# Kernel tuning notes

Hardware: AMD Instinct MI355X
Metric: run time of the kernel (lower is better)

The kernel has to match this reference:

```python
import jax, jax.numpy as jnp
import numpy as np

P = 8.0  # Lp norm order for NormDist layers (finite-p distance conv)
CHUNK = 8  # output-channel chunk for memory-bounded distance computation
EPS = 8.0 / 255.0


def lp_norm(d, p=P):
    # stable Lp norm over last axis: m * (sum((d/m)^p))^(1/p)
    m = jnp.max(d, axis=-1)
    ms = jnp.where(m > 0, m, 1.0)
    s = jnp.sum((d / ms[..., None]) ** p, axis=-1)
    ss = jnp.where(m > 0, s, 1.0)
    return m * ss ** (1.0 / p)


def extract_patches(t, k, s, pad):
    # [B,C,H,W] -> [B, L, C*k*k] (torch-unfold channel-major ordering), L=Ho*Wo
    pt = jax.lax.conv_general_dilated_patches(t, (k, k), (s, s), [(pad, pad), (pad, pad)])
    B, F, Ho, Wo = pt.shape
    return pt.reshape(B, F, Ho * Wo).transpose(0, 2, 1), Ho, Wo


def normdist_conv(c, lo, hi, w, k, s, pad):
    # Lp-distance conv with interval bound propagation on (center, lower, upper)
    pc, Ho, Wo = extract_patches(c, k, s, pad)
    pl, _, _ = extract_patches(lo, k, s, pad)
    ph, _, _ = extract_patches(hi, k, s, pad)
    O = w.shape[0]
    wf = w.reshape(O, -1)  # [O, F]

    def per_chunk(wc):  # wc: [CHUNK, F]
        dc = jnp.abs(pc[:, :, None, :] - wc)                     # [B,L,CHUNK,F]
        oc = lp_norm(dc)
        # per-element distance bounds given lo <= x <= hi
        dl = jnp.maximum(jnp.maximum(pl[:, :, None, :] - wc, wc - ph[:, :, None, :]), 0.0)
        ol = lp_norm(dl)
        dh = jnp.maximum(jnp.abs(pl[:, :, None, :] - wc), jnp.abs(ph[:, :, None, :] - wc))
        oh = lp_norm(dh)
        return oc, ol, oh

    oc, ol, oh = jax.lax.map(per_chunk, wf.reshape(O // CHUNK, CHUNK, -1))

    def to_img(t):  # [nch, B, L, CHUNK] -> [B, O, Ho, Wo]
        nch, B, L, ch = t.shape
        return t.transpose(1, 0, 3, 2).reshape(B, nch * ch, Ho, Wo)

    return to_img(oc), to_img(ol), to_img(oh)


def bound_relu(c, lo, hi):
    return jax.nn.relu(c), jax.nn.relu(lo), jax.nn.relu(hi)


def _mp(t):
    return jax.lax.reduce_window(t, -jnp.inf, jax.lax.max, (1, 1, 3, 3), (1, 1, 2, 2), 'VALID')


def bound_maxpool(c, lo, hi):
    return _mp(c), _mp(lo), _mp(hi)


def bound_linear(c, lo, hi, W, b=None):
    oc = c @ W.T
    mid = ((lo + hi) * 0.5) @ W.T
    rad = ((hi - lo) * 0.5) @ jnp.abs(W).T
    if b is not None:
        oc = oc + b
        mid = mid + b
    return oc, mid - rad, mid + rad


def setup_inputs() -> dict:
    key = jax.random.key(0)
    ks = jax.random.split(key, 10)
    x = jax.random.normal(ks[0], (16, 3, 32, 32), jnp.float32)
    lower = x - EPS
    upper = x + EPS
    w1 = jax.random.normal(ks[1], (96, 3, 7, 7), jnp.float32)
    w2 = jax.random.normal(ks[2], (256, 96, 5, 5), jnp.float32)
    w3 = jax.random.normal(ks[3], (384, 256, 3, 3), jnp.float32)
    w4 = jax.random.normal(ks[4], (384, 384, 3, 3), jnp.float32)
    w5 = jax.random.normal(ks[5], (256, 384, 3, 3), jnp.float32)
    fw1 = jax.random.normal(ks[6], (1024, 2304), jnp.float32) * 0.02
    fw2 = jax.random.normal(ks[7], (512, 1024), jnp.float32) * 0.03
    fw3 = jax.random.normal(ks[8], (10, 512), jnp.float32) * 0.04
    fb3 = jax.random.normal(ks[9], (10,), jnp.float32)
    return {"x": x, "lower": lower, "upper": upper, "w1": w1, "w2": w2, "w3": w3,
            "w4": w4, "w5": w5, "fw1": fw1, "fw2": fw2, "fw3": fw3, "fb3": fb3}


def reference(x, lower, upper, w1, w2, w3, w4, w5, fw1, fw2, fw3, fb3):
    c, l, u = normdist_conv(x, lower, upper, w1, 7, 2, 2)   # 32 -> 15
    c, l, u = bound_relu(c, l, u)
    c, l, u = bound_maxpool(c, l, u)                        # 15 -> 7
    c, l, u = normdist_conv(c, l, u, w2, 5, 1, 2)           # 7 -> 7
    c, l, u = bound_relu(c, l, u)
    c, l, u = bound_maxpool(c, l, u)                        # 7 -> 3
    c, l, u = normdist_conv(c, l, u, w3, 3, 1, 1)
    c, l, u = bound_relu(c, l, u)
    c, l, u = normdist_conv(c, l, u, w4, 3, 1, 1)
    c, l, u = bound_relu(c, l, u)
    c, l, u = normdist_conv(c, l, u, w5, 3, 1, 1)
    c, l, u = bound_relu(c, l, u)
    B = c.shape[0]
    c, l, u = c.reshape(B, -1), l.reshape(B, -1), u.reshape(B, -1)
    c, l, u = bound_linear(c, l, u, fw1)
    c, l, u = bound_relu(c, l, u)
    c, l, u = bound_linear(c, l, u, fw2)
    c, l, u = bound_relu(c, l, u)
    c, l, u = bound_linear(c, l, u, fw3, fb3)
    # final negation swaps the roles of lower/upper
    return (-c, -u, -l)
```

## Files before the change

### kernel.cpp

```cpp
#include <hip/hip_runtime.h>
#include <math.h>


typedef float vf2 __attribute__((ext_vector_type(2)));

__device__ __forceinline__ float rt8(float s) { return sqrtf(sqrtf(sqrtf(s))); }

__device__ __forceinline__ void tap16(float w, float pc, float pl, float pu,
                                      float& aC, float& aL, float& aH)
{
    float a = pc - w; float a2 = a * a, a4 = a2 * a2; aC = fmaf(a4, a4, aC);
    float x = pl - w, y = pu - w;
    float dl = fmaxf(fmaxf(x, -y), 0.f);
    float e2 = dl * dl, e4 = e2 * e2; aL = fmaf(e4, e4, aL);
    float h2 = fmaxf(x * x, y * y);
    float h4 = h2 * h2; aH = fmaf(h4, h4, aH);
}

__device__ __forceinline__ void tap16v2(vf2 w, vf2 pc, vf2 pl, vf2 pu,
                                        vf2& aC, vf2& aL, vf2& aH)
{
    vf2 a = pc - w; vf2 a2 = a * a, a4 = a2 * a2;
    aC = __builtin_elementwise_fma(a4, a4, aC);
    vf2 x = pl - w, y = pu - w;
    vf2 zero = {0.f, 0.f};
    vf2 dl = __builtin_elementwise_max(__builtin_elementwise_max(x, -y), zero);
    vf2 e2 = dl * dl, e4 = e2 * e2;
    aL = __builtin_elementwise_fma(e4, e4, aL);
    vf2 h2 = __builtin_elementwise_max(x * x, y * y);
    vf2 h4 = h2 * h2;
    aH = __builtin_elementwise_fma(h4, h4, aH);
}

__launch_bounds__(256)
__global__ void prep_kernel(const float* __restrict__ W2, const float* __restrict__ W3,
                            const float* __restrict__ W4, const float* __restrict__ W5,
                            float* __restrict__ T2, float* __restrict__ T3,
                            float* __restrict__ T4, float* __restrict__ T5,
                            const float* __restrict__ IC, const float* __restrict__ IL,
                            const float* __restrict__ IU, const float* __restrict__ W1,
                            float* __restrict__ A)
{
    constexpr int nt2 = 152, nt3 = 216, nt4 = 324, nt5 = 216;
    constexpr int NTW = nt2 + nt3 + nt4 + nt5;
    __shared__ float u[3 * 3 * 1225];
    int bid = blockIdx.x;
    int tid = threadIdx.x;

    if (bid < NTW) {
        const float* W; float* T; int O, CK, KK, t;
        if (bid < nt2)                  { W = W2; T = T2; O = 256; CK = 2400; KK = 25; t = bid; }
        else if (bid < nt2 + nt3)       { W = W3; T = T3; O = 384; CK = 2304; KK = 9; t = bid - nt2; }
        else if (bid < nt2 + nt3 + nt4) { W = W4; T = T4; O = 384; CK = 3456; KK = 9; t = bid - nt2 - nt3; }
        else                            { W = W5; T = T5; O = 256; CK = 3456; KK = 9; t = bid - nt2 - nt3 - nt4; }
        int tilesC = (CK + 63) / 64;
        int to = t / tilesC, tc = t - to * tilesC;
        int o0 = to * 64, c0 = tc * 64;
        int lane = tid & 63, wv = tid >> 6;
        #pragma unroll
        for (int i = 0; i < 16; ++i) {
            int row = wv + i * 4;
            int c = c0 + lane;
            u[row * 65 + lane] = (c < CK) ? W[(size_t)(o0 + row) * CK + c] : 0.f;
        }
        __syncthreads();
        #pragma unroll
        for (int i = 0; i < 16; ++i) {
            int row = wv + i * 4;
            int ck = c0 + row;
            if (ck < CK) {
                int c = ck / KK, tt = ck - c * KK;
                T[(size_t)((c >> 1) * KK + tt) * (2 * O) + (size_t)(o0 + lane) * 2 + (c & 1)]
                    = u[lane * 65 + row];
            }
        }
        return;
    }

    constexpr int PP = 1225, PW = 35, HW = 1024;
    int t = bid - NTW;
    int og = t % 24; t /= 24;
    int b  = t % 16; int r = t / 16;

    for (int i = tid; i < 3 * 3 * PP; i += 256) u[i] = 0.f;
    __syncthreads();
    for (int tsel = 0; tsel < 3; ++tsel) {
        const float* src = (tsel == 0 ? IC : (tsel == 1 ? IL : IU)) + (size_t)b * 3 * HW;
        for (int e = tid; e < 3 * HW; e += 256) {
            int c = e / HW, p = e % HW;
            int pr = p / 32, pw_ = p % 32;
            u[c * 3 * PP + tsel * PP + (pr + 2) * PW + (pw_ + 2)] = src[e];
        }
    }
    __syncthreads();

    int wave = tid >> 6, lane = tid & 63;
    int o = og * 4 + wave;
    const float* wp = W1 + (size_t)o * 147;
    int pos = r * 64 + lane;
    if (pos < 225) {
        int oh = pos / 15, ow = pos % 15;
        const float* sl = u + (oh * 2) * PW + ow * 2;
        float aC = 0.f, aL = 0.f, aH = 0.f;
        #pragma unroll
        for (int c = 0; c < 3; ++c) {
            #pragma unroll
            for (int kh = 0; kh < 7; ++kh)
                #pragma unroll
                for (int kw = 0; kw < 7; ++kw) {
                    float w = wp[c * 49 + kh * 7 + kw];
                    tap16(w, sl[kh * PW + kw], sl[PP + kh * PW + kw],
                          sl[2 * PP + kh * PW + kw], aC, aL, aH);
                }
            sl += 3 * PP;
        }
        size_t N = (size_t)16 * 96 * 225;
        size_t oi = ((size_t)b * 96 + o) * 225 + pos;
        A[oi] = aC; A[N + oi] = aL; A[2 * N + oi] = aH;
    }
}

template<int CC>
__launch_bounds__(256)
__global__ void conv2_kernel(const float* __restrict__ A, const float* __restrict__ WT,
                             float* __restrict__ P)
{
    constexpr int B = 16, Cin = 96, O = 256;
    constexpr int CP = CC / 2;
    constexpr size_t N = (size_t)B * O * 49;
    constexpr size_t NA = (size_t)B * 96 * 225;
    __shared__ __align__(16) float slab[CP * 360];
    int x = blockIdx.x;
    int oh   = x % 7;
    int b    = (x / 7) % B;
    int chunk = x / (7 * B);
    int c0 = chunk * CC;
    int tid = threadIdx.x;

    for (int i = tid; i < CP * 360; i += 256) {
        int cp = i / 360; int rem = i - cp * 360;
        int tsel = rem / 120; int rr = rem - tsel * 120;
        int r = rr / 24; int cpar = rr - r * 24;
        int col = cpar >> 1, par = cpar & 1;
        int c = c0 + cp * 2 + par;
        int ih = oh + r - 2, iw = col - 2;
        float v = 0.f;
        if (col < 11 && (unsigned)ih < 7u && (unsigned)iw < 7u) {
            const float* ap = A + (size_t)tsel * NA + ((size_t)b * 96 + c) * 225
                            + (ih * 2) * 15 + iw * 2;
            float m = 0.f;
            #pragma unroll
            for (int pi = 0; pi < 3; ++pi)
                #pragma unroll
                for (int pj = 0; pj < 3; ++pj)
                    m = fmaxf(m, ap[pi * 15 + pj]);
            v = rt8(m);
        }
        slab[i] = v;
    }
    __syncthreads();

    int o = tid;
    vf2 aC2[7], aL2[7], aH2[7];
    vf2 zero = {0.f, 0.f};
    #pragma unroll
    for (int u = 0; u < 7; ++u) { aC2[u] = zero; aL2[u] = zero; aH2[u] = zero; }

    for (int cp = 0; cp < CP; ++cp) {
        const float* wp = WT + (size_t)((c0 / 2 + cp) * 25) * (2 * O) + 2 * o;
        const float* sb = slab + cp * 360;
        #pragma unroll
        for (int r = 0; r < 5; ++r) {
            vf2 wr[5];
            #pragma unroll
            for (int kw = 0; kw < 5; ++kw)
                wr[kw] = *(const vf2*)(wp + (size_t)(r * 5 + kw) * (2 * O));
            vf2 X[12], L[12], U[12];
            #pragma unroll
            for (int i2 = 0; i2 < 12; ++i2) {
                X[i2] = *(const vf2*)(sb + r * 24 + i2 * 2);
                L[i2] = *(const vf2*)(sb + 120 + r * 24 + i2 * 2);
                U[i2] = *(const vf2*)(sb + 240 + r * 24 + i2 * 2);
            }
            #pragma unroll
            for (int ow = 0; ow < 7; ++ow)
                #pragma unroll
                for (int kw = 0; kw < 5; ++kw)
                    tap16v2(wr[kw], X[ow + kw], L[ow + kw], U[ow + kw],
                            aC2[ow], aL2[ow], aH2[ow]);
        }
    }

    float* Pc = P + (size_t)chunk * 3 * N;
    size_t rowbase = ((size_t)(b * 7 + oh) * 7) * O + o;
    #pragma unroll
    for (int u = 0; u < 7; ++u) {
        Pc[rowbase + (size_t)u * O]         = aC2[u].x + aC2[u].y;
        Pc[N + rowbase + (size_t)u * O]     = aL2[u].x + aL2[u].y;
        Pc[2 * N + rowbase + (size_t)u * O] = aH2[u].x + aH2[u].y;
    }
}

__global__ void comb2_pool2(const float* __restrict__ P, float* __restrict__ D)
{
    constexpr int B = 16, O = 256, NCH = 16;
    constexpr size_t N = (size_t)B * O * 49;
    int idx = blockIdx.x * blockDim.x + threadIdx.x;
    if (idx >= 3 * B * 9 * O) return;
    int o = idx & 255; int t = idx >> 8;
    int pos = t % 9; t /= 9;
    int b = t % B; int tsel = t / B;
    int ph = pos / 3, pw = pos % 3;
    float m = 0.f;
    #pragma unroll
    for (int i = 0; i < 3; ++i)
        #pragma unroll
        for (int j = 0; j < 3; ++j) {
            int sp = (ph * 2 + i) * 7 + (pw * 2 + j);
            size_t base = (size_t)tsel * N + ((size_t)b * 49 + sp) * O + o;
            float s = 0.f;
            #pragma unroll
            for (int ch = 0; ch < NCH; ++ch) s += P[(size_t)ch * 3 * N + base];
            m = fmaxf(m, s);
        }
    D[idx] = rt8(m);
}

template<int CC, int NCHIN>
__launch_bounds__(384)
__global__ void conv3x3_kernel(const float* __restrict__ IN, const float* __restrict__ WT,
                               float* __restrict__ P, int B, int Cin, int O)
{
    constexpr int CP = CC / 2;
    __shared__ __align__(8) float slab[CP * 150];
    int x = blockIdx.x;
    int b = x % B;
    int chunk = x / B;
    int c0 = chunk * CC;
    int tid = threadIdx.x;

    size_t NN = (size_t)B * Cin * 9;
    for (int i = tid; i < CP * 150; i += blockDim.x) {
        int cp = i / 150; int rem = i - cp * 150;
        int tsel = rem / 50; int rr = rem - tsel * 50;
        int p = rr >> 1, par = rr & 1;
        int iy = p / 5, ix = p - iy * 5;
        int ih = iy - 1, iw = ix - 1;
        int c = c0 + cp * 2 + par;
        float v = 0.f;
        if ((unsigned)ih < 3u && (unsigned)iw < 3u) {
            size_t base = (size_t)tsel * NN + ((size_t)b * 9 + (ih * 3 + iw)) * Cin + c;
            if (NCHIN == 0) {
                v = IN[base];
            } else {
                float s = 0.f;
                #pragma unroll 8
                for (int ch = 0; ch < NCHIN; ++ch) s += IN[(size_t)ch * 3 * NN + base];
                v = rt8(s);
            }
        }
        slab[i] = v;
    }
    __syncthreads();

    int o = tid;
    vf2 aC2[9], aL2[9], aH2[9];
    vf2 zero = {0.f, 0.f};
    #pragma unroll
    for (int u = 0; u < 9; ++u) { aC2[u] = zero; aL2[u] = zero; aH2[u] = zero; }

    for (int cp = 0; cp < CP; ++cp) {
        const float* wp = WT + (size_t)((c0 / 2 + cp) * 9) * (2 * O) + 2 * o;
        vf2 w2[9];
        #pragma unroll
        for (int t = 0; t < 9; ++t) w2[t] = *(const vf2*)(wp + (size_t)t * (2 * O));
        const float* sb = slab + cp * 150;
        #pragma unroll
        for (int py = 0; py < 3; ++py)
            #pragma unroll
            for (int px = 0; px < 3; ++px)
                #pragma unroll
                for (int ky = 0; ky < 3; ++ky)
                    #pragma unroll
                    for (int kx = 0; kx < 3; ++kx) {
                        int p = (py + ky) * 5 + (px + kx);
                        tap16v2(w2[ky * 3 + kx],
                                *(const vf2*)(sb + p * 2),
                                *(const vf2*)(sb + 50 + p * 2),
                                *(const vf2*)(sb + 100 + p * 2),
                                aC2[py * 3 + px], aL2[py * 3 + px], aH2[py * 3 + px]);
                    }
    }

    size_t N = (size_t)B * O * 9;
    float* Pc = P + (size_t)chunk * 3 * N;
    size_t base = ((size_t)b * 9) * O + o;
    #pragma unroll
    for (int u = 0; u < 9; ++u) {
        Pc[base + (size_t)u * O]         = aC2[u].x + aC2[u].y;
        Pc[N + base + (size_t)u * O]     = aL2[u].x + aL2[u].y;
        Pc[2 * N + base + (size_t)u * O] = aH2[u].x + aH2[u].y;
    }
}

__global__ void comb5_std(const float* __restrict__ P, float* __restrict__ G, int NCH)
{
    constexpr int B = 16, O = 256;
    constexpr size_t N = (size_t)B * O * 9;
    size_t idx = (size_t)blockIdx.x * blockDim.x + threadIdx.x;
    if (idx >= 3 * N) return;
    float s = 0.f;
    for (int ch = 0; ch < NCH; ++ch) s += P[(size_t)ch * 3 * N + idx];
    int o = (int)(idx % O); size_t t = idx / O;
    int pos = (int)(t % 9); t /= 9;
    int b = (int)(t % B); int tsel = (int)(t / B);
    G[(size_t)tsel * N + ((size_t)b * O + o) * 9 + pos] = rt8(s);
}

__launch_bounds__(256)
__global__ void fc_gemv(const float* __restrict__ IC, const float* __restrict__ IL,
                        const float* __restrict__ IU, const float* __restrict__ W,
                        float* __restrict__ OUT, int B, int In, int Out)
{
    int gw = (int)((blockIdx.x * blockDim.x + threadIdx.x) >> 6);
    int lane = threadIdx.x & 63;
    if (gw >= B * Out) return;
    int o = gw % Out, b = gw / Out;
    const float4* wr = (const float4*)(W  + (size_t)o * In);
    const float4* cr = (const float4*)(IC + (size_t)b * In);
    const float4* lr = (const float4*)(IL + (size_t)b * In);
    const float4* ur = (const float4*)(IU + (size_t)b * In);
    int In4 = In >> 2;
    float sc = 0.f, sm = 0.f, sr = 0.f;
    for (int i = lane; i < In4; i += 64) {
        float4 w4 = wr[i], c4 = cr[i], l4 = lr[i], u4 = ur[i];
        sc = fmaf(c4.x, w4.x, sc); sc = fmaf(c4.y, w4.y, sc);
        sc = fmaf(c4.z, w4.z, sc); sc = fmaf(c4.w, w4.w, sc);
        sm = fmaf((l4.x + u4.x) * 0.5f, w4.x, sm);
        sm = fmaf((l4.y + u4.y) * 0.5f, w4.y, sm);
        sm = fmaf((l4.z + u4.z) * 0.5f, w4.z, sm);
        sm = fmaf((l4.w + u4.w) * 0.5f, w4.w, sm);
        sr = fmaf((u4.x - l4.x) * 0.5f, fabsf(w4.x), sr);
        sr = fmaf((u4.y - l4.y) * 0.5f, fabsf(w4.y), sr);
        sr = fmaf((u4.z - l4.z) * 0.5f, fabsf(w4.z), sr);
        sr = fmaf((u4.w - l4.w) * 0.5f, fabsf(w4.w), sr);
    }
    #pragma unroll
    for (int off = 32; off; off >>= 1) {
        sc += __shfl_xor(sc, off);
        sm += __shfl_xor(sm, off);
        sr += __shfl_xor(sr, off);
    }
    if (lane == 0) {
        size_t N = (size_t)B * Out;
        size_t idx = (size_t)b * Out + o;
        OUT[idx]         = fmaxf(sc, 0.f);
        OUT[N + idx]     = fmaxf(sm - sr, 0.f);
        OUT[2 * N + idx] = fmaxf(sm + sr, 0.f);
    }
}

__global__ void bound_linear_kernel(
    const float* __restrict__ IC, const float* __restrict__ IL, const float* __restrict__ IU,
    const float* __restrict__ W, const float* __restrict__ bias,
    float* __restrict__ OC, float* __restrict__ OL, float* __restrict__ OU,
    int B, int In, int Out)
{
    int idx = blockIdx.x * blockDim.x + threadIdx.x;
    if (idx >= B * Out) return;
    int o = idx % Out, b = idx / Out;
    const float* wr = W  + (size_t)o * In;
    const float* cr = IC + (size_t)b * In;
    const float* lr = IL + (size_t)b * In;
    const float* ur = IU + (size_t)b * In;
    float sc = 0.f, sm = 0.f, sr = 0.f;
    for (int i = 0; i < In; ++i) {
        float w = wr[i];
        sc = fmaf(cr[i], w, sc);
        sm = fmaf((lr[i] + ur[i]) * 0.5f, w, sm);
        sr = fmaf((ur[i] - lr[i]) * 0.5f, fabsf(w), sr);
    }
    float bb = bias[o]; sc += bb; sm += bb;
    OC[idx] = -sc; OL[idx] = -(sm - sr); OU[idx] = -(sm + sr);
}

extern "C" void kernel_launch(void* const* d_in, const int* in_sizes, int n_in,
                              void* d_out, int out_size, void* d_ws, size_t ws_size,
                              hipStream_t stream)
{
    const float* x   = (const float*)d_in[0];
    const float* lo  = (const float*)d_in[1];
    const float* hi  = (const float*)d_in[2];
    const float* w1  = (const float*)d_in[3];
    const float* w2  = (const float*)d_in[4];
    const float* w3  = (const float*)d_in[5];
    const float* w4  = (const float*)d_in[6];
    const float* w5  = (const float*)d_in[7];
    const float* fw1 = (const float*)d_in[8];
    const float* fw2 = (const float*)d_in[9];
    const float* fw3 = (const float*)d_in[10];
    const float* fb3 = (const float*)d_in[11];
    float* out = (float*)d_out;
    float* ws  = (float*)d_ws;

    const size_t n_c1 = 16u * 96 * 225;
    const size_t n_d  = 16u * 256 * 9;
    const size_t n_c5 = 16u * 256 * 9;
    const size_t n_f1 = 16u * 1024;
    const size_t n_f2 = 16u * 512;
    const size_t N3   = 16u * 384 * 9;

    float* A   = ws;
    float* D   = A  + 3 * n_c1;
    float* G   = D  + 3 * n_d;
    float* H   = G  + 3 * n_c5;
    float* I   = H  + 3 * n_f1;
    float* WT2 = I  + 3 * n_f2;
    float* WT3 = WT2 + 614400;
    float* WT4 = WT3 + 884736;
    float* WT5 = WT4 + 1327104;
    float* SP2 = WT5 + 884736;
    float* SPa = SP2;
    float* SPc = SP2;
    float* SPb = SP2 + 32u * 3 * N3;

    const int BS = 256;
    auto grid = [](size_t tot) { return dim3((unsigned)((tot + 255) / 256)); };

    prep_kernel<<<908 + 1536, BS, 0, stream>>>(
        w2, w3, w4, w5, WT2, WT3, WT4, WT5, x, lo, hi, w1, A);
    conv2_kernel<6><<<16 * 16 * 7, 256, 0, stream>>>(A, WT2, SP2);
    comb2_pool2<<<grid(3 * n_d), BS, 0, stream>>>(SP2, D);
    conv3x3_kernel<8, 0><<<32 * 16, 384, 0, stream>>>(D, WT3, SPa, 16, 256, 384);
    conv3x3_kernel<8, 32><<<48 * 16, 384, 0, stream>>>(SPa, WT4, SPb, 16, 384, 384);
    conv3x3_kernel<8, 48><<<48 * 16, 256, 0, stream>>>(SPb, WT5, SPc, 16, 384, 256);
    comb5_std<<<grid(3 * n_c5), BS, 0, stream>>>(SPc, G, 48);
    fc_gemv<<<grid(16384u * 64), BS, 0, stream>>>(
        G, G + n_c5, G + 2 * n_c5, fw1, H, 16, 2304, 1024);
    fc_gemv<<<grid(8192u * 64), BS, 0, stream>>>(
        H, H + n_f1, H + 2 * n_f1, fw2, I, 16, 1024, 512);
    bound_linear_kernel<<<grid(160), BS, 0, stream>>>(
        I, I + n_f2, I + 2 * n_f2, fw3, fb3,
        out, out + 320, out + 160, 16, 512, 10);
}
```

Before: 582.5 us.

## Fuse pool into conv3, register-tile 3x3 slab, batch FC gemv, retune conv2 chunks

```diff
diff --git a/kernel.cpp b/kernel.cpp
--- a/kernel.cpp
+++ b/kernel.cpp
@@ -201,38 +201,29 @@
     }
 }
 
-__global__ void comb2_pool2(const float* __restrict__ P, float* __restrict__ D)
-{
-    constexpr int B = 16, O = 256, NCH = 16;
-    constexpr size_t N = (size_t)B * O * 49;
-    int idx = blockIdx.x * blockDim.x + threadIdx.x;
-    if (idx >= 3 * B * 9 * O) return;
-    int o = idx & 255; int t = idx >> 8;
-    int pos = t % 9; t /= 9;
-    int b = t % B; int tsel = t / B;
-    int ph = pos / 3, pw = pos % 3;
-    float m = 0.f;
-    #pragma unroll
-    for (int i = 0; i < 3; ++i)
-        #pragma unroll
-        for (int j = 0; j < 3; ++j) {
-            int sp = (ph * 2 + i) * 7 + (pw * 2 + j);
-            size_t base = (size_t)tsel * N + ((size_t)b * 49 + sp) * O + o;
-            float s = 0.f;
-            #pragma unroll
-            for (int ch = 0; ch < NCH; ++ch) s += P[(size_t)ch * 3 * N + base];
-            m = fmaxf(m, s);
-        }
-    D[idx] = rt8(m);
-}
-
-template<int CC, int NCHIN>
+#define LDROW(R, off, iy) { \
+    float4 q0 = *(const float4*)(sb + (off) + (iy) * 12); \
+    float4 q1 = *(const float4*)(sb + (off) + (iy) * 12 + 4); \
+    vf2   q2 = *(const vf2*)(sb + (off) + (iy) * 12 + 8); \
+    R[iy][0] = vf2{q0.x, q0.y}; R[iy][1] = vf2{q0.z, q0.w}; \
+    R[iy][2] = vf2{q1.x, q1.y}; R[iy][3] = vf2{q1.z, q1.w}; \
+    R[iy][4] = q2; }
+
+#define TAPS(py) \
+    _Pragma("unroll") for (int px = 0; px < 3; ++px) \
+    _Pragma("unroll") for (int ky = 0; ky < 3; ++ky) \
+    _Pragma("unroll") for (int kx = 0; kx < 3; ++kx) \
+        tap16v2(w2[ky * 3 + kx], X[(py) + ky][px + kx], L[(py) + ky][px + kx], \
+                U[(py) + ky][px + kx], aC2[(py) * 3 + px], aL2[(py) * 3 + px], \
+                aH2[(py) * 3 + px]);
+
+template<int CC, int NCHIN, bool POOL>
 __launch_bounds__(384)
 __global__ void conv3x3_kernel(const float* __restrict__ IN, const float* __restrict__ WT,
                                float* __restrict__ P, int B, int Cin, int O)
 {
     constexpr int CP = CC / 2;
-    __shared__ __align__(8) float slab[CP * 150];
+    __shared__ __align__(16) float slab[CP * 180];
     int x = blockIdx.x;
     int b = x % B;
     int chunk = x / B;
@@ -240,19 +231,34 @@
     int tid = threadIdx.x;
 
     size_t NN = (size_t)B * Cin * 9;
-    for (int i = tid; i < CP * 150; i += blockDim.x) {
-        int cp = i / 150; int rem = i - cp * 150;
-        int tsel = rem / 50; int rr = rem - tsel * 50;
-        int p = rr >> 1, par = rr & 1;
-        int iy = p / 5, ix = p - iy * 5;
-        int ih = iy - 1, iw = ix - 1;
+    constexpr size_t N2 = (size_t)16 * 256 * 49;
+    for (int i = tid; i < CP * 180; i += blockDim.x) {
+        int cp = i / 180; int rem = i - cp * 180;
+        int tsel = rem / 60; int rr = rem - tsel * 60;
+        int iy = rr / 12; int cc2 = rr - iy * 12;
+        int col = cc2 >> 1, par = cc2 & 1;
+        int ih = iy - 1, iw = col - 1;
         int c = c0 + cp * 2 + par;
         float v = 0.f;
         if ((unsigned)ih < 3u && (unsigned)iw < 3u) {
-            size_t base = (size_t)tsel * NN + ((size_t)b * 9 + (ih * 3 + iw)) * Cin + c;
-            if (NCHIN == 0) {
-                v = IN[base];
+            if (POOL) {
+                float m = 0.f;
+                #pragma unroll
+                for (int pi = 0; pi < 3; ++pi)
+                    #pragma unroll
+                    for (int pj = 0; pj < 3; ++pj) {
+                        int sp = (ih * 2 + pi) * 7 + (iw * 2 + pj);
+                        size_t base = (size_t)tsel * N2 + ((size_t)b * 49 + sp) * 256 + c;
+                        float s = 0.f;
+                        #pragma unroll
+                        for (int ch = 0; ch < 12; ++ch) s += IN[(size_t)ch * 3 * N2 + base];
+                        m = fmaxf(m, s);
+                    }
+                v = rt8(m);
+            } else if (NCHIN == 0) {
+                v = IN[(size_t)tsel * NN + ((size_t)b * 9 + (ih * 3 + iw)) * Cin + c];
             } else {
+                size_t base = (size_t)tsel * NN + ((size_t)b * 9 + (ih * 3 + iw)) * Cin + c;
                 float s = 0.f;
                 #pragma unroll 8
                 for (int ch = 0; ch < NCHIN; ++ch) s += IN[(size_t)ch * 3 * NN + base];
@@ -274,22 +280,16 @@
         vf2 w2[9];
         #pragma unroll
         for (int t = 0; t < 9; ++t) w2[t] = *(const vf2*)(wp + (size_t)t * (2 * O));
-        const float* sb = slab + cp * 150;
-        #pragma unroll
-        for (int py = 0; py < 3; ++py)
-            #pragma unroll
-            for (int px = 0; px < 3; ++px)
-                #pragma unroll
-                for (int ky = 0; ky < 3; ++ky)
-                    #pragma unroll
-                    for (int kx = 0; kx < 3; ++kx) {
-                        int p = (py + ky) * 5 + (px + kx);
-                        tap16v2(w2[ky * 3 + kx],
-                                *(const vf2*)(sb + p * 2),
-                                *(const vf2*)(sb + 50 + p * 2),
-                                *(const vf2*)(sb + 100 + p * 2),
-                                aC2[py * 3 + px], aL2[py * 3 + px], aH2[py * 3 + px]);
-                    }
+        const float* sb = slab + cp * 180;
+        vf2 X[5][5], L[5][5], U[5][5];
+        LDROW(X, 0, 0) LDROW(L, 60, 0) LDROW(U, 120, 0)
+        LDROW(X, 0, 1) LDROW(L, 60, 1) LDROW(U, 120, 1)
+        LDROW(X, 0, 2) LDROW(L, 60, 2) LDROW(U, 120, 2)
+        TAPS(0)
+        LDROW(X, 0, 3) LDROW(L, 60, 3) LDROW(U, 120, 3)
+        TAPS(1)
+        LDROW(X, 0, 4) LDROW(L, 60, 4) LDROW(U, 120, 4)
+        TAPS(2)
     }
 
     size_t N = (size_t)B * O * 9;
@@ -318,45 +318,64 @@
 }
 
 __launch_bounds__(256)
-__global__ void fc_gemv(const float* __restrict__ IC, const float* __restrict__ IL,
-                        const float* __restrict__ IU, const float* __restrict__ W,
-                        float* __restrict__ OUT, int B, int In, int Out)
-{
+__global__ void fc_gemv4(const float* __restrict__ IC, const float* __restrict__ IL,
+                         const float* __restrict__ IU, const float* __restrict__ W,
+                         float* __restrict__ OUT, int In, int Out)
+{
+    constexpr int B = 16;
     int gw = (int)((blockIdx.x * blockDim.x + threadIdx.x) >> 6);
     int lane = threadIdx.x & 63;
-    if (gw >= B * Out) return;
-    int o = gw % Out, b = gw / Out;
-    const float4* wr = (const float4*)(W  + (size_t)o * In);
-    const float4* cr = (const float4*)(IC + (size_t)b * In);
-    const float4* lr = (const float4*)(IL + (size_t)b * In);
-    const float4* ur = (const float4*)(IU + (size_t)b * In);
+    if (gw >= Out * 4) return;
+    int o = gw % Out, bg = gw / Out;
+    int b0 = bg * 4;
+    const float4* wr = (const float4*)(W + (size_t)o * In);
+    const float4* cr[4]; const float4* lr[4]; const float4* ur[4];
+    #pragma unroll
+    for (int q = 0; q < 4; ++q) {
+        cr[q] = (const float4*)(IC + (size_t)(b0 + q) * In);
+        lr[q] = (const float4*)(IL + (size_t)(b0 + q) * In);
+        ur[q] = (const float4*)(IU + (size_t)(b0 + q) * In);
+    }
     int In4 = In >> 2;
-    float sc = 0.f, sm = 0.f, sr = 0.f;
+    float sc[4] = {0.f, 0.f, 0.f, 0.f};
+    float sm[4] = {0.f, 0.f, 0.f, 0.f};
+    float sr[4] = {0.f, 0.f, 0.f, 0.f};
     for (int i = lane; i < In4; i += 64) {
-        float4 w4 = wr[i], c4 = cr[i], l4 = lr[i], u4 = ur[i];
-        sc = fmaf(c4.x, w4.x, sc); sc = fmaf(c4.y, w4.y, sc);
-        sc = fmaf(c4.z, w4.z, sc); sc = fmaf(c4.w, w4.w, sc);
-        sm = fmaf((l4.x + u4.x) * 0.5f, w4.x, sm);
-        sm = fmaf((l4.y + u4.y) * 0.5f, w4.y, sm);
-        sm = fmaf((l4.z + u4.z) * 0.5f, w4.z, sm);
-        sm = fmaf((l4.w + u4.w) * 0.5f, w4.w, sm);
-        sr = fmaf((u4.x - l4.x) * 0.5f, fabsf(w4.x), sr);
-        sr = fmaf((u4.y - l4.y) * 0.5f, fabsf(w4.y), sr);
-        sr = fmaf((u4.z - l4.z) * 0.5f, fabsf(w4.z), sr);
-        sr = fmaf((u4.w - l4.w) * 0.5f, fabsf(w4.w), sr);
+        float4 w4 = wr[i];
+        float ax = fabsf(w4.x), ay = fabsf(w4.y), az = fabsf(w4.z), aw = fabsf(w4.w);
+        #pragma unroll
+        for (int q = 0; q < 4; ++q) {
+            float4 c4 = cr[q][i], l4 = lr[q][i], u4 = ur[q][i];
+            sc[q] = fmaf(c4.x, w4.x, sc[q]); sc[q] = fmaf(c4.y, w4.y, sc[q]);
+            sc[q] = fmaf(c4.z, w4.z, sc[q]); sc[q] = fmaf(c4.w, w4.w, sc[q]);
+            sm[q] = fmaf((l4.x + u4.x) * 0.5f, w4.x, sm[q]);
+            sm[q] = fmaf((l4.y + u4.y) * 0.5f, w4.y, sm[q]);
+            sm[q] = fmaf((l4.z + u4.z) * 0.5f, w4.z, sm[q]);
+            sm[q] = fmaf((l4.w + u4.w) * 0.5f, w4.w, sm[q]);
+            sr[q] = fmaf((u4.x - l4.x) * 0.5f, ax, sr[q]);
+            sr[q] = fmaf((u4.y - l4.y) * 0.5f, ay, sr[q]);
+            sr[q] = fmaf((u4.z - l4.z) * 0.5f, az, sr[q]);
+            sr[q] = fmaf((u4.w - l4.w) * 0.5f, aw, sr[q]);
+        }
     }
     #pragma unroll
     for (int off = 32; off; off >>= 1) {
-        sc += __shfl_xor(sc, off);
-        sm += __shfl_xor(sm, off);
-        sr += __shfl_xor(sr, off);
+        #pragma unroll
+        for (int q = 0; q < 4; ++q) {
+            sc[q] += __shfl_xor(sc[q], off);
+            sm[q] += __shfl_xor(sm[q], off);
+            sr[q] += __shfl_xor(sr[q], off);
+        }
     }
     if (lane == 0) {
         size_t N = (size_t)B * Out;
-        size_t idx = (size_t)b * Out + o;
-        OUT[idx]         = fmaxf(sc, 0.f);
-        OUT[N + idx]     = fmaxf(sm - sr, 0.f);
-        OUT[2 * N + idx] = fmaxf(sm + sr, 0.f);
+        #pragma unroll
+        for (int q = 0; q < 4; ++q) {
+            size_t idx = (size_t)(b0 + q) * Out + o;
+            OUT[idx]         = fmaxf(sc[q], 0.f);
+            OUT[N + idx]     = fmaxf(sm[q] - sr[q], 0.f);
+            OUT[2 * N + idx] = fmaxf(sm[q] + sr[q], 0.f);
+        }
     }
 }
 
@@ -404,15 +423,13 @@
     float* ws  = (float*)d_ws;
 
     const size_t n_c1 = 16u * 96 * 225;
-    const size_t n_d  = 16u * 256 * 9;
     const size_t n_c5 = 16u * 256 * 9;
     const size_t n_f1 = 16u * 1024;
     const size_t n_f2 = 16u * 512;
     const size_t N3   = 16u * 384 * 9;
 
     float* A   = ws;
-    float* D   = A  + 3 * n_c1;
-    float* G   = D  + 3 * n_d;
+    float* G   = A  + 3 * n_c1;
     float* H   = G  + 3 * n_c5;
     float* I   = H  + 3 * n_f1;
     float* WT2 = I  + 3 * n_f2;
@@ -420,25 +437,24 @@
     float* WT4 = WT3 + 884736;
     float* WT5 = WT4 + 1327104;
     float* SP2 = WT5 + 884736;
-    float* SPa = SP2;
-    float* SPc = SP2;
-    float* SPb = SP2 + 32u * 3 * N3;
+    float* SPb = SP2;
+    float* SPa = SP2 + 48u * 3 * N3;
+    float* SPc = SPa;
 
     const int BS = 256;
     auto grid = [](size_t tot) { return dim3((unsigned)((tot + 255) / 256)); };
 
     prep_kernel<<<908 + 1536, BS, 0, stream>>>(
         w2, w3, w4, w5, WT2, WT3, WT4, WT5, x, lo, hi, w1, A);
-    conv2_kernel<6><<<16 * 16 * 7, 256, 0, stream>>>(A, WT2, SP2);
-    comb2_pool2<<<grid(3 * n_d), BS, 0, stream>>>(SP2, D);
-    conv3x3_kernel<8, 0><<<32 * 16, 384, 0, stream>>>(D, WT3, SPa, 16, 256, 384);
-    conv3x3_kernel<8, 32><<<48 * 16, 384, 0, stream>>>(SPa, WT4, SPb, 16, 384, 384);
-    conv3x3_kernel<8, 48><<<48 * 16, 256, 0, stream>>>(SPb, WT5, SPc, 16, 384, 256);
+    conv2_kernel<8><<<12 * 16 * 7, 256, 0, stream>>>(A, WT2, SP2);
+    conv3x3_kernel<8, 0, true><<<32 * 16, 384, 0, stream>>>(SP2, WT3, SPa, 16, 256, 384);
+    conv3x3_kernel<8, 32, false><<<48 * 16, 384, 0, stream>>>(SPa, WT4, SPb, 16, 384, 384);
+    conv3x3_kernel<8, 48, false><<<48 * 16, 256, 0, stream>>>(SPb, WT5, SPc, 16, 384, 256);
     comb5_std<<<grid(3 * n_c5), BS, 0, stream>>>(SPc, G, 48);
-    fc_gemv<<<grid(16384u * 64), BS, 0, stream>>>(
-        G, G + n_c5, G + 2 * n_c5, fw1, H, 16, 2304, 1024);
-    fc_gemv<<<grid(8192u * 64), BS, 0, stream>>>(
-        H, H + n_f1, H + 2 * n_f1, fw2, I, 16, 1024, 512);
+    fc_gemv4<<<grid(4096u * 64), BS, 0, stream>>>(
+        G, G + n_c5, G + 2 * n_c5, fw1, H, 2304, 1024);
+    fc_gemv4<<<grid(2048u * 64), BS, 0, stream>>>(
+        H, H + n_f1, H + 2 * n_f1, fw2, I, 1024, 512);
     bound_linear_kernel<<<grid(160), BS, 0, stream>>>(
         I, I + n_f2, I + 2 * n_f2, fw3, fb3,
         out, out + 320, out + 160, 16, 512, 10);
```

Result: slower. 603.2 us (+3.5%).
